# Kernel optimization log

Hardware: AMD Instinct MI355X
Metric: run time of the kernel (lower is better)

Reference implementation:

```python
import jax, jax.numpy as jnp
import numpy as np

B, U, V, E, D, L4 = 64, 1024, 1024, 512, 640, 4 * 640


def setup_inputs() -> dict:
    key = jax.random.key(0)
    ks = jax.random.split(key, 9)
    return {
        "targets": jax.random.randint(ks[0], (B, U), 0, V),
        "target_lens": jax.random.randint(ks[1], (B,), 1, U + 1),
        "embed": jax.random.normal(ks[2], (V, E), dtype=jnp.float32) * 0.02,
        "W0": jax.random.normal(ks[3], (E, L4), dtype=jnp.float32) * 0.04,
        "U0": jax.random.normal(ks[4], (D, L4), dtype=jnp.float32) * 0.04,
        "b0": jnp.zeros((L4,), dtype=jnp.float32),
        "W1": jax.random.normal(ks[5], (D, L4), dtype=jnp.float32) * 0.04,
        "U1": jax.random.normal(ks[6], (D, L4), dtype=jnp.float32) * 0.04,
        "b1": jnp.zeros((L4,), dtype=jnp.float32),
    }


def _masked_lstm(x, mask, W, Uw, b):
    """Keras-semantics masked LSTM (i,f,g,o gate order). x:[B,T,in], mask:[B,T].
    Masked steps carry state/output forward (Keras RNN mask behavior)."""
    d = Uw.shape[0]
    xz = jnp.einsum('bti,ig->btg', x, W) + b  # precompute input projection [B,T,4D]

    def step(carry, inp):
        h, c = carry
        z_t, m = inp  # [B,4D], [B]
        z = z_t + h @ Uw
        i, f, g, o = jnp.split(z, 4, axis=-1)
        i = jax.nn.sigmoid(i)
        f = jax.nn.sigmoid(f)
        g = jnp.tanh(g)
        o = jax.nn.sigmoid(o)
        c_new = f * c + i * g
        h_new = o * jnp.tanh(c_new)
        m = m[:, None]
        h2 = jnp.where(m, h_new, h)
        c2 = jnp.where(m, c_new, c)
        return (h2, c2), h2

    h0 = jnp.zeros((x.shape[0], d), dtype=x.dtype)
    (_, _), ys = jax.lax.scan(step, (h0, h0), (xz.transpose(1, 0, 2), mask.T))
    return ys.transpose(1, 0, 2)  # [B,T,D]


def reference(targets, target_lens, embed, W0, U0, b0, W1, U1, b1):
    x = embed[targets]  # [B,U,E]
    mask = jnp.arange(targets.shape[1])[None, :] < target_lens[:, None]  # [B,U]
    x = _masked_lstm(x, mask, W0, U0, b0)
    x = _masked_lstm(x, mask, W1, U1, b1)
    return x
```

## Files before the change

kernel.cpp:

```cpp
#include <hip/hip_runtime.h>
#include <math.h>

#define B_   64
#define U_   1024
#define E_   512
#define D_   640
#define L4_  2560
#define TC   64
#define NCH  16
#define NBLK 160
#define SUBQ (NBLK / 8)

template <int MODE>
__global__ __launch_bounds__(256) void gemm_kernel(
    const float* __restrict__ A,
    const int*   __restrict__ targets,
    const float* __restrict__ Wm,
    const float* __restrict__ bias,
    float* __restrict__ xz,
    int K, int t0)
{
    const int tid = threadIdx.x;
    const int m0 = blockIdx.x * 128;
    const int n0 = blockIdx.y * 128;

    __shared__ float As[8][132];
    __shared__ float Bs[8][132];

    float acc[8][8];
#pragma unroll
    for (int i = 0; i < 8; ++i)
#pragma unroll
        for (int j = 0; j < 8; ++j) acc[i][j] = 0.f;

    const float* a_ptr;
    int a_ml = 0, a_kq = 0, a_k = 0;
    if (MODE == 0) {
        a_ml = tid & 127;
        a_kq = (tid >> 7) * 4;
        int m  = m0 + a_ml;
        int b  = m & 63;
        int tl = m >> 6;
        int idx = targets[b * U_ + t0 + tl];
        a_ptr = A + (size_t)idx * E_ + a_kq;
    } else {
        a_k  = tid >> 5;
        a_ml = (tid & 31) * 4;
        int m  = m0 + a_ml;
        int b  = m & 63;
        int tl = m >> 6;
        a_ptr = A + (size_t)tl * (D_ * 64) + (size_t)a_k * 64 + b;
    }
    const int b_k  = tid >> 5;
    const int b_n4 = (tid & 31) * 4;

    const int tx = tid & 15;
    const int ty = tid >> 4;

    for (int k0 = 0; k0 < K; k0 += 8) {
        if (MODE == 0) {
            float4 av = *(const float4*)(a_ptr + k0);
            As[a_kq + 0][a_ml] = av.x;
            As[a_kq + 1][a_ml] = av.y;
            As[a_kq + 2][a_ml] = av.z;
            As[a_kq + 3][a_ml] = av.w;
        } else {
            float4 av = *(const float4*)(a_ptr + (size_t)k0 * 64);
            *(float4*)&As[a_k][a_ml] = av;
        }
        {
            float4 bv = *(const float4*)(Wm + (size_t)(k0 + b_k) * L4_ + n0 + b_n4);
            *(float4*)&Bs[b_k][b_n4] = bv;
        }
        __syncthreads();

#pragma unroll
        for (int k = 0; k < 8; ++k) {
            float af[8], bf[8];
            *(float4*)&af[0] = *(const float4*)&As[k][ty * 8];
            *(float4*)&af[4] = *(const float4*)&As[k][ty * 8 + 4];
            *(float4*)&bf[0] = *(const float4*)&Bs[k][tx * 8];
            *(float4*)&bf[4] = *(const float4*)&Bs[k][tx * 8 + 4];
#pragma unroll
            for (int i = 0; i < 8; ++i)
#pragma unroll
                for (int j = 0; j < 8; ++j) acc[i][j] += af[i] * bf[j];
        }
        __syncthreads();
    }

#pragma unroll
    for (int i = 0; i < 8; ++i) {
        int m  = m0 + ty * 8 + i;
        int tl = m >> 6;
        int b  = m & 63;
        float* outp = xz + (size_t)tl * (L4_ * 64) + b;
#pragma unroll
        for (int j = 0; j < 8; ++j) {
            int n = n0 + tx * 8 + j;
            outp[(size_t)n * 64] = acc[i][j] + bias[n];
        }
    }
}

__global__ __launch_bounds__(256) void prep_up_kernel(
    const float* __restrict__ U0w, const float* __restrict__ U1w,
    float* __restrict__ Up0, float* __restrict__ Up1)
{
    const int k = blockIdx.x;
    const float* Uw = blockIdx.y ? U1w : U0w;
    float*       Up = blockIdx.y ? Up1 : Up0;
    for (int d = threadIdx.x; d < D_; d += 256) {
        const int g  = d >> 2;
        const int dd = d & 3;
#pragma unroll
        for (int gate = 0; gate < 4; ++gate) {
            float v = Uw[(size_t)k * L4_ + gate * 640 + d];
            Up[((size_t)g * 16 + dd * 4 + gate) * 640 + k] = v;
        }
    }
}

__device__ __forceinline__ float ldg_llc(const float* p) {
    return __hip_atomic_load(p, __ATOMIC_RELAXED, __HIP_MEMORY_SCOPE_AGENT);
}
__device__ __forceinline__ unsigned long long ldg_llc2(const unsigned long long* p) {
    return __hip_atomic_load(p, __ATOMIC_RELAXED, __HIP_MEMORY_SCOPE_AGENT);
}
__device__ __forceinline__ void stg_llc(float* p, float v) {
    __hip_atomic_store(p, v, __ATOMIC_RELAXED, __HIP_MEMORY_SCOPE_AGENT);
}

__device__ __forceinline__ void grid_barrier(unsigned* bar, unsigned done)
{
    asm volatile("s_waitcnt vmcnt(0)" ::: "memory");
    __syncthreads();
    if (threadIdx.x == 0) {
        unsigned* sub    = bar + ((blockIdx.x & 7) << 5);
        unsigned* master = bar + (8 << 5);
        unsigned a = __hip_atomic_fetch_add(sub, 1u, __ATOMIC_RELAXED, __HIP_MEMORY_SCOPE_AGENT);
        if (a == done * SUBQ - 1u)
            __hip_atomic_fetch_add(master, 1u, __ATOMIC_RELAXED, __HIP_MEMORY_SCOPE_AGENT);
        const unsigned tgt = done * 8u;
        while (__hip_atomic_load(master, __ATOMIC_RELAXED, __HIP_MEMORY_SCOPE_AGENT) < tgt)
            __builtin_amdgcn_s_sleep(1);
    }
    __syncthreads();
}

__global__ __launch_bounds__(256) void lstm_seq_kernel(
    const float* __restrict__ xz,
    const float* __restrict__ Upg,
    float* __restrict__ hA,
    float* __restrict__ hB,
    float* __restrict__ c_st,
    const int* __restrict__ lens,
    float* __restrict__ hc_out,
    int t0,
    unsigned* __restrict__ bar,
    unsigned bar_base)
{
    const int tid  = threadIdx.x;
    const int d0   = blockIdx.x * 4;
    const int ks   = tid >> 6;
    const int kbeg = ks * 160;
    const int lane   = tid & 63;
    const int n_base = (lane >> 5) * 8;
    const int b_grp  = lane & 31;
    const int b0     = b_grp * 2;

    __shared__ float U_lds[16 * 640];
    __shared__ float red[64][64];

    {
        const float* upg = Upg + (size_t)blockIdx.x * (640 * 16);
#pragma unroll
        for (int it = 0; it < 10; ++it) {
            const int e = (it * 256 + tid) * 4;
            *(float4*)&U_lds[e] = *(const float4*)(upg + e);
        }
    }

    const int ed = d0 + (tid >> 6);
    const int eb = tid & 63;
    float c_reg   = c_st[ed * 64 + eb];
    const int len_b = lens[eb];

    __syncthreads();

    float acc[16];
    unsigned long long HAb[16], HBb[16];
    float UAb[32], UBb[32];

#define HLOADB(HH, KK)                                                      \
    _Pragma("unroll")                                                       \
    for (int j = 0; j < 16; ++j)                                            \
        HH[j] = ldg_llc2(hull + ((KK) + j) * 32 + b_grp);

#define ULOADB(UU, KK)                                                      \
    _Pragma("unroll")                                                       \
    for (int i = 0; i < 8; ++i)                                             \
        *(float4*)&UU[i * 4] =                                              \
            *(const float4*)&U_lds[(n_base + i) * 640 + kbeg + (KK)];

#define FMAS(HH, S, UU)                                                     \
    _Pragma("unroll")                                                       \
    for (int jk = 0; jk < 4; ++jk) {                                        \
        const unsigned long long hu = HH[(S) * 4 + jk];                     \
        const float hlo = __uint_as_float((unsigned)hu);                    \
        const float hhi = __uint_as_float((unsigned)(hu >> 32));            \
        _Pragma("unroll")                                                   \
        for (int i = 0; i < 8; ++i) {                                       \
            const float uv = UU[i * 4 + jk];                                \
            acc[i * 2 + 0] += uv * hlo;                                     \
            acc[i * 2 + 1] += uv * hhi;                                     \
        }                                                                   \
    }

#pragma unroll 1
    for (int tl = 0; tl < TC; ++tl) {
        const int t = t0 + tl;
        const float* hp = (t & 1) ? hB : hA;
        float*       hn = (t & 1) ? hA : hB;

        float xzv[4];
        {
            const float* xzp = xz + (size_t)tl * (L4_ * 64) + eb;
#pragma unroll
            for (int g = 0; g < 4; ++g)
                xzv[g] = xzp[(size_t)(ed + 640 * g) * 64];
        }
        const float hp_epi = ldg_llc(hp + ed * 64 + eb);

#pragma unroll
        for (int i = 0; i < 16; ++i) acc[i] = 0.f;

        const unsigned long long* hull =
            (const unsigned long long*)hp + (size_t)kbeg * 32;

        HLOADB(HAb, 0)
        ULOADB(UAb, 0)
#pragma unroll
        for (int tt = 0; tt < 5; ++tt) {
            const int kb = tt * 32;
            HLOADB(HBb, kb + 16)
            ULOADB(UBb, kb + 4);   FMAS(HAb, 0, UAb)
            ULOADB(UAb, kb + 8);   FMAS(HAb, 1, UBb)
            ULOADB(UBb, kb + 12);  FMAS(HAb, 2, UAb)
            ULOADB(UAb, kb + 16);  FMAS(HAb, 3, UBb)
            if (tt < 4) { HLOADB(HAb, kb + 32) }
            ULOADB(UBb, kb + 20);  FMAS(HBb, 0, UAb)
            ULOADB(UAb, kb + 24);  FMAS(HBb, 1, UBb)
            ULOADB(UBb, kb + 28);  FMAS(HBb, 2, UAb)
            if (tt < 4) { ULOADB(UAb, kb + 32) }
            FMAS(HBb, 3, UBb)
        }

#pragma unroll
        for (int i = 0; i < 8; ++i)
            *(float2*)&red[((n_base + i) << 2) | ks][b0] =
                make_float2(acc[i * 2], acc[i * 2 + 1]);
        __syncthreads();

        {
            const int dd = tid >> 6;
            float z[4];
#pragma unroll
            for (int g = 0; g < 4; ++g) {
                const int r = ((dd * 4 + g) << 2);
                z[g] = red[r][eb] + red[r + 1][eb] + red[r + 2][eb] + red[r + 3][eb]
                     + xzv[g];
            }
            float ig = 1.f / (1.f + __expf(-z[0]));
            float fg = 1.f / (1.f + __expf(-z[1]));
            float gg = tanhf(z[2]);
            float og = 1.f / (1.f + __expf(-z[3]));
            float c_new = fg * c_reg + ig * gg;
            float h_new = og * tanhf(c_new);
            bool msk = t < len_b;
            float h_out = msk ? h_new : hp_epi;
            c_reg = msk ? c_new : c_reg;
            stg_llc(hn + ed * 64 + eb, h_out);
            hc_out[(size_t)tl * (D_ * 64) + ed * 64 + eb] = h_out;
        }

        if (tl != TC - 1)
            grid_barrier(bar, bar_base + (unsigned)tl + 1u);
    }
    c_st[ed * 64 + eb] = c_reg;
#undef HLOADB
#undef ULOADB
#undef FMAS
}

__global__ __launch_bounds__(256) void transpose_kernel(
    const float* __restrict__ h1c, float* __restrict__ out, int t0)
{
    const int tl   = blockIdx.x;
    const int dblk = blockIdx.y;
    __shared__ float tile[64][65];

    const int r  = threadIdx.x >> 2;
    const int cq = threadIdx.x & 3;

    const float* src = h1c + (size_t)tl * (D_ * 64) + (size_t)(dblk * 64 + r) * 64 + cq * 16;
#pragma unroll
    for (int j = 0; j < 4; ++j) {
        float4 v = *(const float4*)(src + j * 4);
        tile[r][cq * 16 + j * 4 + 0] = v.x;
        tile[r][cq * 16 + j * 4 + 1] = v.y;
        tile[r][cq * 16 + j * 4 + 2] = v.z;
        tile[r][cq * 16 + j * 4 + 3] = v.w;
    }
    __syncthreads();

    float* dst = out + (size_t)r * (U_ * D_) + (size_t)(t0 + tl) * D_ + dblk * 64 + cq * 16;
#pragma unroll
    for (int j = 0; j < 4; ++j) {
        float4 w;
        w.x = tile[cq * 16 + j * 4 + 0][r];
        w.y = tile[cq * 16 + j * 4 + 1][r];
        w.z = tile[cq * 16 + j * 4 + 2][r];
        w.w = tile[cq * 16 + j * 4 + 3][r];
        *(float4*)(dst + j * 4) = w;
    }
}

extern "C" void kernel_launch(void* const* d_in, const int* in_sizes, int n_in,
                              void* d_out, int out_size, void* d_ws, size_t ws_size,
                              hipStream_t stream)
{
    const int*   targets = (const int*)d_in[0];
    const int*   lens    = (const int*)d_in[1];
    const float* embed   = (const float*)d_in[2];
    const float* W0      = (const float*)d_in[3];
    const float* U0      = (const float*)d_in[4];
    const float* b0      = (const float*)d_in[5];
    const float* W1      = (const float*)d_in[6];
    const float* U1      = (const float*)d_in[7];
    const float* b1      = (const float*)d_in[8];
    float* out = (float*)d_out;
    float* ws  = (float*)d_ws;

    float* xz  = ws;
    float* h0c = xz  + (size_t)TC * L4_ * 64;
    float* h1c = h0c + (size_t)TC * D_ * 64;
    float* st  = h1c + (size_t)TC * D_ * 64;
    float* h0a = st;
    float* h0b = st + 40960;
    float* c0  = st + 2 * 40960;
    float* h1a = st + 3 * 40960;
    float* h1b = st + 4 * 40960;
    float* c1  = st + 5 * 40960;
    unsigned* bar = (unsigned*)(st + 6 * 40960);
    float* Up0 = st + 6 * 40960 + 512;
    float* Up1 = Up0 + (size_t)D_ * L4_;

    hipMemsetAsync(st, 0, (size_t)6 * 40960 * sizeof(float) + 2048, stream);

    prep_up_kernel<<<dim3(D_, 2), dim3(256), 0, stream>>>(U0, U1, Up0, Up1);

    const dim3 gemm_grid(TC * 64 / 128, L4_ / 128);
    const dim3 blk(256);

    unsigned launch_idx = 0;
    for (int ch = 0; ch < NCH; ++ch) {
        const int t0 = ch * TC;

        gemm_kernel<0><<<gemm_grid, blk, 0, stream>>>(embed, targets, W0, b0, xz, E_, t0);

        lstm_seq_kernel<<<dim3(NBLK), blk, 0, stream>>>(
            xz, Up0, h0a, h0b, c0, lens, h0c, t0, bar, launch_idx * 63u);
        ++launch_idx;

        gemm_kernel<1><<<gemm_grid, blk, 0, stream>>>(h0c, targets, W1, b1, xz, D_, t0);

        lstm_seq_kernel<<<dim3(NBLK), blk, 0, stream>>>(
            xz, Up1, h1a, h1b, c1, lens, h1c, t0, bar, launch_idx * 63u);
        ++launch_idx;

        transpose_kernel<<<dim3(TC, 10), blk, 0, stream>>>(h1c, out, t0);
    }
}
```

Baseline: 25.10 ms.

## Remap LSTM recurrent matvec tiling and read h state straight from output buffer

The recurrent step's thread mapping is reworked so each thread computes 2 gate rows by 8 batch columns. It uses float4 loads of h, a triple-buffered load/FMA pipeline, and a padded LDS pitch for the U weights to avoid bank conflicts. The ping-pong h buffers are removed: each step reads the previous hidden state from the per-step output slab with plain loads instead of agent-scope atomic loads, and stores h only once. Because every step writes fresh addresses, stale cached lines should not be an issue, but this relies on the grid barrier's memory ordering.

```diff
diff --git a/kernel.cpp b/kernel.cpp
--- a/kernel.cpp
+++ b/kernel.cpp
@@ -10,6 +10,7 @@
 #define NCH  16
 #define NBLK 160
 #define SUBQ (NBLK / 8)
+#define UPITCH 644
 
 template <int MODE>
 __global__ __launch_bounds__(256) void gemm_kernel(
@@ -121,12 +122,6 @@
     }
 }
 
-__device__ __forceinline__ float ldg_llc(const float* p) {
-    return __hip_atomic_load(p, __ATOMIC_RELAXED, __HIP_MEMORY_SCOPE_AGENT);
-}
-__device__ __forceinline__ unsigned long long ldg_llc2(const unsigned long long* p) {
-    return __hip_atomic_load(p, __ATOMIC_RELAXED, __HIP_MEMORY_SCOPE_AGENT);
-}
 __device__ __forceinline__ void stg_llc(float* p, float v) {
     __hip_atomic_store(p, v, __ATOMIC_RELAXED, __HIP_MEMORY_SCOPE_AGENT);
 }
@@ -151,8 +146,7 @@
 __global__ __launch_bounds__(256) void lstm_seq_kernel(
     const float* __restrict__ xz,
     const float* __restrict__ Upg,
-    float* __restrict__ hA,
-    float* __restrict__ hB,
+    const float* __restrict__ hinit,
     float* __restrict__ c_st,
     const int* __restrict__ lens,
     float* __restrict__ hc_out,
@@ -165,19 +159,21 @@
     const int ks   = tid >> 6;
     const int kbeg = ks * 160;
     const int lane   = tid & 63;
-    const int n_base = (lane >> 5) * 8;
-    const int b_grp  = lane & 31;
-    const int b0     = b_grp * 2;
-
-    __shared__ float U_lds[16 * 640];
+    const int n_base = (lane >> 3) * 2;
+    const int b0     = (lane & 7) * 8;
+
+    __shared__ float U_lds[16 * UPITCH];
     __shared__ float red[64][64];
 
     {
-        const float* upg = Upg + (size_t)blockIdx.x * (640 * 16);
+        const float4* upg = (const float4*)(Upg + (size_t)blockIdx.x * (640 * 16));
+        float4* udst = (float4*)U_lds;
 #pragma unroll
         for (int it = 0; it < 10; ++it) {
-            const int e = (it * 256 + tid) * 4;
-            *(float4*)&U_lds[e] = *(const float4*)(upg + e);
+            const int e = it * 256 + tid;
+            const int r = e / 160;
+            const int c = e - r * 160;
+            udst[r * (UPITCH / 4) + c] = upg[e];
         }
     }
 
@@ -189,39 +185,37 @@
     __syncthreads();
 
     float acc[16];
-    unsigned long long HAb[16], HBb[16];
-    float UAb[32], UBb[32];
-
-#define HLOADB(HH, KK)                                                      \
+    float HA[32], HB[32], HC[32];
+    float UA[8],  UB[8],  UC[8];
+
+#define HLOAD(HH)                                                           \
     _Pragma("unroll")                                                       \
-    for (int j = 0; j < 16; ++j)                                            \
-        HH[j] = ldg_llc2(hull + ((KK) + j) * 32 + b_grp);
-
-#define ULOADB(UU, KK)                                                      \
+    for (int j = 0; j < 4; ++j) {                                           \
+        *(float4*)&HH[j * 8 + 0] = *(const float4*)(hrun + j * 64);         \
+        *(float4*)&HH[j * 8 + 4] = *(const float4*)(hrun + j * 64 + 4);     \
+    }                                                                       \
+    hrun += 256;
+
+#define ULOAD(UU)                                                           \
+    *(float4*)&UU[0] = *(const float4*)(urun);                              \
+    *(float4*)&UU[4] = *(const float4*)(urun + UPITCH);                     \
+    urun += 4;
+
+#define FMAG(HH, UU)                                                        \
     _Pragma("unroll")                                                       \
-    for (int i = 0; i < 8; ++i)                                             \
-        *(float4*)&UU[i * 4] =                                              \
-            *(const float4*)&U_lds[(n_base + i) * 640 + kbeg + (KK)];
-
-#define FMAS(HH, S, UU)                                                     \
-    _Pragma("unroll")                                                       \
-    for (int jk = 0; jk < 4; ++jk) {                                        \
-        const unsigned long long hu = HH[(S) * 4 + jk];                     \
-        const float hlo = __uint_as_float((unsigned)hu);                    \
-        const float hhi = __uint_as_float((unsigned)(hu >> 32));            \
+    for (int j = 0; j < 4; ++j)                                             \
         _Pragma("unroll")                                                   \
-        for (int i = 0; i < 8; ++i) {                                       \
-            const float uv = UU[i * 4 + jk];                                \
-            acc[i * 2 + 0] += uv * hlo;                                     \
-            acc[i * 2 + 1] += uv * hhi;                                     \
-        }                                                                   \
-    }
+        for (int i = 0; i < 2; ++i)                                         \
+            _Pragma("unroll")                                               \
+            for (int q = 0; q < 8; ++q)                                     \
+                acc[i * 8 + q] += UU[i * 4 + j] * HH[j * 8 + q];
 
 #pragma unroll 1
     for (int tl = 0; tl < TC; ++tl) {
         const int t = t0 + tl;
-        const float* hp = (t & 1) ? hB : hA;
-        float*       hn = (t & 1) ? hA : hB;
+        const float* hprev = (tl == 0) ? hinit
+                           : hc_out + (size_t)(tl - 1) * (D_ * 64);
+        float*       hcur  = hc_out + (size_t)tl * (D_ * 64);
 
         float xzv[4];
         {
@@ -230,36 +224,33 @@
             for (int g = 0; g < 4; ++g)
                 xzv[g] = xzp[(size_t)(ed + 640 * g) * 64];
         }
-        const float hp_epi = ldg_llc(hp + ed * 64 + eb);
+        const float hp_epi = hprev[ed * 64 + eb];
 
 #pragma unroll
         for (int i = 0; i < 16; ++i) acc[i] = 0.f;
 
-        const unsigned long long* hull =
-            (const unsigned long long*)hp + (size_t)kbeg * 32;
-
-        HLOADB(HAb, 0)
-        ULOADB(UAb, 0)
-#pragma unroll
-        for (int tt = 0; tt < 5; ++tt) {
-            const int kb = tt * 32;
-            HLOADB(HBb, kb + 16)
-            ULOADB(UBb, kb + 4);   FMAS(HAb, 0, UAb)
-            ULOADB(UAb, kb + 8);   FMAS(HAb, 1, UBb)
-            ULOADB(UBb, kb + 12);  FMAS(HAb, 2, UAb)
-            ULOADB(UAb, kb + 16);  FMAS(HAb, 3, UBb)
-            if (tt < 4) { HLOADB(HAb, kb + 32) }
-            ULOADB(UBb, kb + 20);  FMAS(HBb, 0, UAb)
-            ULOADB(UAb, kb + 24);  FMAS(HBb, 1, UBb)
-            ULOADB(UBb, kb + 28);  FMAS(HBb, 2, UAb)
-            if (tt < 4) { ULOADB(UAb, kb + 32) }
-            FMAS(HBb, 3, UBb)
-        }
-
-#pragma unroll
-        for (int i = 0; i < 8; ++i)
-            *(float2*)&red[((n_base + i) << 2) | ks][b0] =
-                make_float2(acc[i * 2], acc[i * 2 + 1]);
+        const float* hrun = hprev + (size_t)kbeg * 64 + b0;
+        const float* urun = &U_lds[n_base * UPITCH + kbeg];
+
+        HLOAD(HA) ULOAD(UA)
+        HLOAD(HB) ULOAD(UB)
+        HLOAD(HC) ULOAD(UC)
+#pragma unroll 1
+        for (int t3 = 0; t3 < 12; ++t3) {
+            FMAG(HA, UA) HLOAD(HA) ULOAD(UA)
+            FMAG(HB, UB) HLOAD(HB) ULOAD(UB)
+            FMAG(HC, UC) HLOAD(HC) ULOAD(UC)
+        }
+        FMAG(HA, UA) HLOAD(HA) ULOAD(UA)
+        FMAG(HB, UB)
+        FMAG(HC, UC)
+        FMAG(HA, UA)
+
+#pragma unroll
+        for (int i = 0; i < 2; ++i) {
+            *(float4*)&red[((n_base + i) << 2) | ks][b0]     = *(float4*)&acc[i * 8];
+            *(float4*)&red[((n_base + i) << 2) | ks][b0 + 4] = *(float4*)&acc[i * 8 + 4];
+        }
         __syncthreads();
 
         {
@@ -280,17 +271,16 @@
             bool msk = t < len_b;
             float h_out = msk ? h_new : hp_epi;
             c_reg = msk ? c_new : c_reg;
-            stg_llc(hn + ed * 64 + eb, h_out);
-            hc_out[(size_t)tl * (D_ * 64) + ed * 64 + eb] = h_out;
+            stg_llc(hcur + ed * 64 + eb, h_out);
         }
 
         if (tl != TC - 1)
             grid_barrier(bar, bar_base + (unsigned)tl + 1u);
     }
     c_st[ed * 64 + eb] = c_reg;
-#undef HLOADB
-#undef ULOADB
-#undef FMAS
+#undef HLOAD
+#undef ULOAD
+#undef FMAG
 }
 
 __global__ __launch_bounds__(256) void transpose_kernel(
@@ -346,11 +336,8 @@
     float* h0c = xz  + (size_t)TC * L4_ * 64;
     float* h1c = h0c + (size_t)TC * D_ * 64;
     float* st  = h1c + (size_t)TC * D_ * 64;
-    float* h0a = st;
-    float* h0b = st + 40960;
+    float* hzero = st;
     float* c0  = st + 2 * 40960;
-    float* h1a = st + 3 * 40960;
-    float* h1b = st + 4 * 40960;
     float* c1  = st + 5 * 40960;
     unsigned* bar = (unsigned*)(st + 6 * 40960);
     float* Up0 = st + 6 * 40960 + 512;
@@ -366,17 +353,19 @@
     unsigned launch_idx = 0;
     for (int ch = 0; ch < NCH; ++ch) {
         const int t0 = ch * TC;
+        const float* hinit0 = (ch == 0) ? hzero : h0c + (size_t)(TC - 1) * (D_ * 64);
+        const float* hinit1 = (ch == 0) ? hzero : h1c + (size_t)(TC - 1) * (D_ * 64);
 
         gemm_kernel<0><<<gemm_grid, blk, 0, stream>>>(embed, targets, W0, b0, xz, E_, t0);
 
         lstm_seq_kernel<<<dim3(NBLK), blk, 0, stream>>>(
-            xz, Up0, h0a, h0b, c0, lens, h0c, t0, bar, launch_idx * 63u);
+            xz, Up0, hinit0, c0, lens, h0c, t0, bar, launch_idx * 63u);
         ++launch_idx;
 
         gemm_kernel<1><<<gemm_grid, blk, 0, stream>>>(h0c, targets, W1, b1, xz, D_, t0);
 
         lstm_seq_kernel<<<dim3(NBLK), blk, 0, stream>>>(
-            xz, Up1, h1a, h1b, c1, lens, h1c, t0, bar, launch_idx * 63u);
+            xz, Up1, hinit1, c1, lens, h1c, t0, bar, launch_idx * 63u);
         ++launch_idx;
 
         transpose_kernel<<<dim3(TC, 10), blk, 0, stream>>>(h1c, out, t0);
```

New measurement: 28.83 ms. +14.9%, slower.
